# Optimization experiments

Hardware: AMD Instinct MI355X
Metric: run time of the kernel (lower is better)

## Reference

```python
import jax, jax.numpy as jnp
import numpy as np

B, L, DIM = 2, 2048, 2048
N_HEADS, N_KV_HEADS = 32, 8
HEAD_DIM = DIM // N_HEADS  # 64
SCALE = HEAD_DIM ** -0.5


def setup_inputs() -> dict:
    key = jax.random.key(0)
    ks = jax.random.split(key, 6)
    s = 0.02
    x = jax.random.normal(ks[0], (B, L, DIM), dtype=jnp.float32)
    wq = jax.random.normal(ks[1], (N_HEADS * HEAD_DIM, DIM), dtype=jnp.float32) * s
    wk = jax.random.normal(ks[2], (N_KV_HEADS * HEAD_DIM, DIM), dtype=jnp.float32) * s
    wv = jax.random.normal(ks[3], (N_KV_HEADS * HEAD_DIM, DIM), dtype=jnp.float32) * s
    wo = jax.random.normal(ks[4], (DIM, N_HEADS * HEAD_DIM), dtype=jnp.float32) * s
    # standard RoPE frequencies: theta = 10000^(-2i/d), angle = pos * theta
    inv_freq = 1.0 / (10000.0 ** (jnp.arange(0, HEAD_DIM, 2, dtype=jnp.float32) / HEAD_DIM))
    angles = jnp.arange(L, dtype=jnp.float32)[:, None] * inv_freq[None, :]  # [L, HEAD_DIM//2]
    freqs_cos = jnp.cos(angles)
    freqs_sin = jnp.sin(angles)
    # additive causal mask [1, 1, L, L]
    causal = jnp.tril(jnp.ones((L, L), dtype=bool))
    mask = jnp.where(causal, 0.0, -1e9).astype(jnp.float32)[None, None]
    return {"x": x, "wq": wq, "wk": wk, "wv": wv, "wo": wo,
            "freqs_cos": freqs_cos, "freqs_sin": freqs_sin, "mask": mask}


def _apply_rope(t, cos, sin):
    # t: [B, H, L, D]; complex pairing is (even, odd) interleaved along D
    te, to = t[..., 0::2], t[..., 1::2]
    cos = cos[None, None, : t.shape[2], :]
    sin = sin[None, None, : t.shape[2], :]
    re = te * cos - to * sin
    im = te * sin + to * cos
    return jnp.stack([re, im], axis=-1).reshape(t.shape)


def reference(x, wq, wk, wv, wo, freqs_cos, freqs_sin, mask):
    b, l, _ = x.shape
    q = (x @ wq.T).reshape(b, l, N_HEADS, HEAD_DIM).transpose(0, 2, 1, 3)
    k = (x @ wk.T).reshape(b, l, N_KV_HEADS, HEAD_DIM).transpose(0, 2, 1, 3)
    v = (x @ wv.T).reshape(b, l, N_KV_HEADS, HEAD_DIM).transpose(0, 2, 1, 3)
    q = _apply_rope(q, freqs_cos, freqs_sin)
    k = _apply_rope(k, freqs_cos, freqs_sin)
    repeats = N_HEADS // N_KV_HEADS
    k = jnp.repeat(k, repeats, axis=1)
    v = jnp.repeat(v, repeats, axis=1)
    scores = jnp.einsum("bhqd,bhkd->bhqk", q, k) * SCALE + mask
    probs = jax.nn.softmax(scores, axis=-1)
    out = jnp.einsum("bhqk,bhkd->bhqd", probs, v)
    out = out.transpose(0, 2, 1, 3).reshape(b, l, N_HEADS * HEAD_DIM)
    return out @ wo.T
```

## Files before the change

### kernel.cpp

```cpp
#include <hip/hip_runtime.h>
#include <hip/hip_bf16.h>
#include <stdint.h>

typedef __attribute__((ext_vector_type(8))) short bf16x8;
typedef __attribute__((ext_vector_type(4))) float f32x4;
typedef __attribute__((ext_vector_type(16))) float f32x16;
typedef __attribute__((ext_vector_type(4))) unsigned int u32x4;

#define B_    2
#define L_    2048
#define DIM_  2048
#define NH_   32
#define NKV_  8
#define HD_   64
#define KVD_  512
#define CLOG_ 0.1803368801111244f

__device__ __forceinline__ unsigned short f2bf(float f) {
  unsigned u = __float_as_uint(f);
  u += 0x7fff + ((u >> 16) & 1);
  return (unsigned short)(u >> 16);
}
__device__ __forceinline__ unsigned cvtpk(float lo, float hi_) {
  unsigned r;
  asm("v_cvt_pk_bf16_f32 %0, %1, %2" : "=v"(r) : "v"(lo), "v"(hi_));
  return r;
}

#define GLDS16(gsrc, ldst) __builtin_amdgcn_global_load_lds( \
    (const __attribute__((address_space(1))) unsigned int*)(gsrc), \
    (__attribute__((address_space(3))) unsigned int*)(ldst), 16, 0, 0)

__global__ void cvt_all(const float* __restrict__ x,  const float* __restrict__ wq,
                        const float* __restrict__ wk, const float* __restrict__ wv,
                        const float* __restrict__ wo,
                        unsigned short* __restrict__ xb,  unsigned short* __restrict__ wqb,
                        unsigned short* __restrict__ wkb, unsigned short* __restrict__ wvb,
                        unsigned short* __restrict__ wob) {
  int i = blockIdx.x * blockDim.x + threadIdx.x;
  const float* src; unsigned short* dst; int off;
  if (i < 2097152)      { src = x;  dst = xb;  off = i; }
  else if (i < 3145728) { src = wq; dst = wqb; off = i - 2097152; }
  else if (i < 3407872) { src = wk; dst = wkb; off = i - 3145728; }
  else if (i < 3670016) { src = wv; dst = wvb; off = i - 3407872; }
  else                  { src = wo; dst = wob; off = i - 3670016; }
  float4 v = reinterpret_cast<const float4*>(src)[off];
  ushort4 o;
  o.x = f2bf(v.x); o.y = f2bf(v.y); o.z = f2bf(v.z); o.w = f2bf(v.w);
  reinterpret_cast<ushort4*>(dst)[off] = o;
}

template<int OUT_F32>
__global__ __launch_bounds__(256) void gemm_bt(
    const unsigned short* __restrict__ A,
    const unsigned short* __restrict__ W,
    void* __restrict__ C, int M, int N, int K)
{
  __shared__ unsigned short As[128 * 64];
  __shared__ unsigned short Bs[128 * 64];
  const int tid = threadIdx.x;
  const int lane = tid & 63, wid = tid >> 6;
  const int wm = wid >> 1, wn = wid & 1;
  const int r = lane & 15, g = lane >> 4;
  const int m0 = blockIdx.y * 128, n0 = blockIdx.x * 128;
  f32x4 acc[4][4] = {};
  for (int k0 = 0; k0 < K; k0 += 64) {
#pragma unroll
    for (int p = 0; p < 4; ++p) {
      int off = (p * 256 + tid) * 16;
      int row = off >> 7, colb = off & 127;
      GLDS16((const char*)A + ((size_t)(m0 + row) * K + k0) * 2 + colb,
             (char*)As + off);
      GLDS16((const char*)W + ((size_t)(n0 + row) * K + k0) * 2 + colb,
             (char*)Bs + off);
    }
    __syncthreads();
#pragma unroll
    for (int kk = 0; kk < 2; ++kk) {
      bf16x8 af[4], bfv[4];
#pragma unroll
      for (int i = 0; i < 4; ++i)
        af[i] = *reinterpret_cast<const bf16x8*>(&As[(wm * 64 + i * 16 + r) * 64 + kk * 32 + g * 8]);
#pragma unroll
      for (int i = 0; i < 4; ++i)
        bfv[i] = *reinterpret_cast<const bf16x8*>(&Bs[(wn * 64 + i * 16 + r) * 64 + kk * 32 + g * 8]);
#pragma unroll
      for (int i = 0; i < 4; ++i)
#pragma unroll
        for (int j = 0; j < 4; ++j)
          acc[i][j] = __builtin_amdgcn_mfma_f32_16x16x32_bf16(af[i], bfv[j], acc[i][j], 0, 0, 0);
    }
    __syncthreads();
  }
#pragma unroll
  for (int i = 0; i < 4; ++i)
#pragma unroll
    for (int jf = 0; jf < 4; ++jf)
#pragma unroll
      for (int j = 0; j < 4; ++j) {
        size_t row = (size_t)(m0 + wm * 64 + i * 16 + g * 4 + j);
        size_t col = (size_t)(n0 + wn * 64 + jf * 16 + r);
        float v = acc[i][jf][j];
        if (OUT_F32) ((float*)C)[row * N + col] = v;
        else ((unsigned short*)C)[row * N + col] = f2bf(v);
      }
}

__global__ __launch_bounds__(256) void gemm_qkv(
    const unsigned short* __restrict__ A,
    const unsigned short* __restrict__ Wq,
    const unsigned short* __restrict__ Wk,
    const unsigned short* __restrict__ Wv,
    unsigned short* __restrict__ Cq,
    unsigned short* __restrict__ Ck,
    unsigned short* __restrict__ Cv)
{
  __shared__ unsigned short As[128 * 64];
  __shared__ unsigned short Bs[128 * 64];
  const int tid = threadIdx.x;
  const int lane = tid & 63, wid = tid >> 6;
  const int wm = wid >> 1, wn = wid & 1;
  const int r = lane & 15, g = lane >> 4;
  const int bx = blockIdx.x;
  const unsigned short* W; unsigned short* C; int N, n0;
  if (bx < 16)      { W = Wq; C = Cq; N = 2048; n0 = bx * 128; }
  else if (bx < 20) { W = Wk; C = Ck; N = 512;  n0 = (bx - 16) * 128; }
  else              { W = Wv; C = Cv; N = 512;  n0 = (bx - 20) * 128; }
  const int m0 = blockIdx.y * 128;
  const int K = DIM_;
  f32x4 acc[4][4] = {};
  for (int k0 = 0; k0 < K; k0 += 64) {
#pragma unroll
    for (int p = 0; p < 4; ++p) {
      int off = (p * 256 + tid) * 16;
      int row = off >> 7, colb = off & 127;
      GLDS16((const char*)A + ((size_t)(m0 + row) * K + k0) * 2 + colb,
             (char*)As + off);
      GLDS16((const char*)W + ((size_t)(n0 + row) * K + k0) * 2 + colb,
             (char*)Bs + off);
    }
    __syncthreads();
#pragma unroll
    for (int kk = 0; kk < 2; ++kk) {
      bf16x8 af[4], bfv[4];
#pragma unroll
      for (int i = 0; i < 4; ++i)
        af[i] = *reinterpret_cast<const bf16x8*>(&As[(wm * 64 + i * 16 + r) * 64 + kk * 32 + g * 8]);
#pragma unroll
      for (int i = 0; i < 4; ++i)
        bfv[i] = *reinterpret_cast<const bf16x8*>(&Bs[(wn * 64 + i * 16 + r) * 64 + kk * 32 + g * 8]);
#pragma unroll
      for (int i = 0; i < 4; ++i)
#pragma unroll
        for (int j = 0; j < 4; ++j)
          acc[i][j] = __builtin_amdgcn_mfma_f32_16x16x32_bf16(af[i], bfv[j], acc[i][j], 0, 0, 0);
    }
    __syncthreads();
  }
#pragma unroll
  for (int i = 0; i < 4; ++i)
#pragma unroll
    for (int jf = 0; jf < 4; ++jf)
#pragma unroll
      for (int j = 0; j < 4; ++j) {
        size_t row = (size_t)(m0 + wm * 64 + i * 16 + g * 4 + j);
        size_t col = (size_t)(n0 + wn * 64 + jf * 16 + r);
        C[row * N + col] = f2bf(acc[i][jf][j]);
      }
}

__global__ void rope_kernel(unsigned short* __restrict__ t,
                            const float* __restrict__ fc,
                            const float* __restrict__ fs, int rowElems,
                            float scale) {
  int p = blockIdx.x * blockDim.x + threadIdx.x;
  int pairsPerRow = rowElems >> 1;
  int row = p / pairsPerRow;
  if (row >= B_ * L_) return;
  int pi = p - row * pairsPerRow;
  int l = row & (L_ - 1);
  int h = pi >> 5, i = pi & 31;
  size_t base = (size_t)row * rowElems + h * 64 + 2 * i;
  float te = __uint_as_float(((unsigned)t[base]) << 16);
  float to = __uint_as_float(((unsigned)t[base + 1]) << 16);
  float c = fc[l * 32 + i] * scale, s = fs[l * 32 + i] * scale;
  t[base]     = f2bf(te * c - to * s);
  t[base + 1] = f2bf(te * s + to * c);
}

__global__ void transpose_v(const unsigned short* __restrict__ V,
                            unsigned short* __restrict__ Vt) {
  __shared__ unsigned short tile[64][65];
  int bkv = blockIdx.y;
  int b = bkv >> 3, kv = bkv & 7;
  int l0 = blockIdx.x * 64;
  int t = threadIdx.x;
#pragma unroll
  for (int it = 0; it < 16; ++it) {
    int idx = it * 256 + t;
    int lr = idx >> 6, dc = idx & 63;
    tile[lr][dc] = V[((size_t)(b * L_) + l0 + lr) * KVD_ + kv * HD_ + dc];
  }
  __syncthreads();
#pragma unroll
  for (int it = 0; it < 16; ++it) {
    int idx = it * 256 + t;
    int dr = idx >> 6, lc = idx & 63;
    Vt[(((size_t)(b * NKV_ + kv)) * HD_ + dr) * L_ + l0 + lc] = tile[lc][dr];
  }
}

__global__ __launch_bounds__(256) void attn_kernel(
    const unsigned short* __restrict__ Q,
    const unsigned short* __restrict__ K,
    const unsigned short* __restrict__ Vt,
    unsigned short* __restrict__ AO)
{
  __shared__ unsigned short Ks[2][64 * 64];
  __shared__ unsigned short Vs[2][64 * 64];
  const int tid = threadIdx.x;
  const int lane = tid & 63, w = tid >> 6;
  const int ql = lane & 31;
  const int hi = lane >> 5;
  const int wid = blockIdx.x;
  const int j = wid >> 6;
  const int blk = j >> 2, pos = j & 3;
  const int base = 15 - 4 * blk;
  const int qt = (blk & 1) ? (base - 3 + pos) : (base - pos);
  const int bh = wid & 63;
  const int b = bh >> 5, h = bh & 31, kv = h >> 2;
  const int q0 = qt * 128;
  const int qw = q0 + w * 32;
  const int nkt = (q0 + 128) >> 6;

  bf16x8 qf[4];
  const unsigned short* qbase = Q + ((size_t)(b * L_ + qw + ql)) * DIM_ + h * HD_ + hi * 8;
#pragma unroll
  for (int dk = 0; dk < 4; ++dk)
    qf[dk] = *reinterpret_cast<const bf16x8*>(qbase + dk * 16);

  const unsigned short* Kg = K + (size_t)b * L_ * KVD_ + kv * HD_;
  const unsigned short* Vg = Vt + ((size_t)(b * NKV_ + kv)) * HD_ * L_;

  f32x16 oacc0 = {}, oacc1 = {};
  float lrow = 0.f;
  const int rsw = (ql & 7) << 4;

  auto STAGE = [&](int buf, int t) {
    const int k0 = t * 64;
#pragma unroll
    for (int p = 0; p < 2; ++p) {
      int off = (p * 256 + tid) * 16;
      int row = off >> 7;
      int colb = (off & 127) ^ ((row & 7) << 4);
      GLDS16((const char*)Kg + ((size_t)(k0 + row)) * (KVD_ * 2) + colb,
             (char*)Ks[buf] + off);
      GLDS16((const char*)Vg + ((size_t)row) * (L_ * 2) + (size_t)k0 * 2 + colb,
             (char*)Vs[buf] + off);
    }
  };

  int cur = 0;
  STAGE(0, 0);
  __syncthreads();

  for (int t = 0; t < nkt; ++t) {
    if (t + 1 < nkt) STAGE(cur ^ 1, t + 1);
    const int k0 = t * 64;
    if (k0 < qw + 32) {
      const char* Kl = (const char*)Ks[cur];
      const char* Vl = (const char*)Vs[cur];
      f32x16 s0 = {}, s1 = {};
      __builtin_amdgcn_s_setprio(1);
#pragma unroll
      for (int dk = 0; dk < 4; ++dk) {
        bf16x8 kf0 = *reinterpret_cast<const bf16x8*>(Kl + ql * 128 + ((dk * 32 + hi * 16) ^ rsw));
        bf16x8 kf1 = *reinterpret_cast<const bf16x8*>(Kl + (32 + ql) * 128 + ((dk * 32 + hi * 16) ^ rsw));
        s0 = __builtin_amdgcn_mfma_f32_32x32x16_bf16(kf0, qf[dk], s0, 0, 0, 0);
        s1 = __builtin_amdgcn_mfma_f32_32x32x16_bf16(kf1, qf[dk], s1, 0, 0, 0);
      }
      __builtin_amdgcn_s_setprio(0);
      float p[32];
      float ps = 0.f;
      if (k0 + 63 > qw) {
        int q = qw + ql;
#pragma unroll
        for (int i = 0; i < 32; ++i) {
          float sv = (i < 16) ? s0[i] : s1[i - 16];
          int kk = k0 + (i >> 4) * 32 + (i & 3) + 8 * ((i & 15) >> 2) + 4 * hi;
          float e = exp2f(sv);
          e = (kk > q) ? 0.f : e;
          p[i] = e; ps += e;
        }
      } else {
#pragma unroll
        for (int i = 0; i < 32; ++i) {
          float sv = (i < 16) ? s0[i] : s1[i - 16];
          p[i] = exp2f(sv); ps += p[i];
        }
      }
      ps += __shfl_xor(ps, 32);
      lrow += ps;
      bf16x8 pf[4];
#pragma unroll
      for (int s = 0; s < 4; ++s) {
        int bp = ((s >> 1) << 4) + ((s & 1) << 3);
        unsigned w0 = cvtpk(p[bp + 0], p[bp + 1]);
        unsigned w1 = cvtpk(p[bp + 2], p[bp + 3]);
        unsigned w2 = cvtpk(p[bp + 4], p[bp + 5]);
        unsigned w3 = cvtpk(p[bp + 6], p[bp + 7]);
        unsigned x0 = (unsigned)__shfl_xor((int)w0, 32);
        unsigned x1 = (unsigned)__shfl_xor((int)w1, 32);
        unsigned x2 = (unsigned)__shfl_xor((int)w2, 32);
        unsigned x3 = (unsigned)__shfl_xor((int)w3, 32);
        u32x4 fw;
        fw[0] = hi ? x2 : w0;
        fw[1] = hi ? x3 : w1;
        fw[2] = hi ? w2 : x0;
        fw[3] = hi ? w3 : x1;
        pf[s] = __builtin_bit_cast(bf16x8, fw);
      }
      __builtin_amdgcn_s_setprio(1);
#pragma unroll
      for (int s = 0; s < 4; ++s) {
        bf16x8 v0 = *reinterpret_cast<const bf16x8*>(Vl + ql * 128 + ((s * 32 + hi * 16) ^ rsw));
        bf16x8 v1 = *reinterpret_cast<const bf16x8*>(Vl + (32 + ql) * 128 + ((s * 32 + hi * 16) ^ rsw));
        oacc0 = __builtin_amdgcn_mfma_f32_32x32x16_bf16(v0, pf[s], oacc0, 0, 0, 0);
        oacc1 = __builtin_amdgcn_mfma_f32_32x32x16_bf16(v1, pf[s], oacc1, 0, 0, 0);
      }
      __builtin_amdgcn_s_setprio(0);
    }
    __syncthreads();
    cur ^= 1;
  }

  float inv = 1.f / lrow;
  unsigned short* obase = AO + ((size_t)(b * L_ + qw + ql)) * DIM_ + h * HD_;
#pragma unroll
  for (int g4 = 0; g4 < 4; ++g4) {
    uint2 u;
    u.x = cvtpk(oacc0[g4 * 4 + 0] * inv, oacc0[g4 * 4 + 1] * inv);
    u.y = cvtpk(oacc0[g4 * 4 + 2] * inv, oacc0[g4 * 4 + 3] * inv);
    *reinterpret_cast<uint2*>(obase + g4 * 8 + hi * 4) = u;
    uint2 v;
    v.x = cvtpk(oacc1[g4 * 4 + 0] * inv, oacc1[g4 * 4 + 1] * inv);
    v.y = cvtpk(oacc1[g4 * 4 + 2] * inv, oacc1[g4 * 4 + 3] * inv);
    *reinterpret_cast<uint2*>(obase + 32 + g4 * 8 + hi * 4) = v;
  }
}

extern "C" void kernel_launch(void* const* d_in, const int* in_sizes, int n_in,
                              void* d_out, int out_size, void* d_ws, size_t ws_size,
                              hipStream_t stream) {
  const float* x  = (const float*)d_in[0];
  const float* wq = (const float*)d_in[1];
  const float* wk = (const float*)d_in[2];
  const float* wv = (const float*)d_in[3];
  const float* wo = (const float*)d_in[4];
  const float* fc = (const float*)d_in[5];
  const float* fs = (const float*)d_in[6];
  float* out = (float*)d_out;

  unsigned short* ws  = (unsigned short*)d_ws;
  unsigned short* xb  = ws;
  unsigned short* wqb = xb  + 8388608;
  unsigned short* wkb = wqb + 4194304;
  unsigned short* wvb = wkb + 1048576;
  unsigned short* wob = wvb + 1048576;
  unsigned short* Qb  = wob + 4194304;
  unsigned short* Kb  = Qb  + 8388608;
  unsigned short* Vb  = Kb  + 2097152;
  unsigned short* Vtb = Vb  + 2097152;
  unsigned short* AOb = Vtb + 2097152;

  cvt_all<<<18432, 256, 0, stream>>>(x, wq, wk, wv, wo, xb, wqb, wkb, wvb, wob);

  gemm_qkv<<<dim3(24, 32), 256, 0, stream>>>(xb, wqb, wkb, wvb, Qb, Kb, Vb);

  rope_kernel<<<16384, 256, 0, stream>>>(Qb, fc, fs, 2048, CLOG_);
  rope_kernel<<<4096,  256, 0, stream>>>(Kb, fc, fs, 512, 1.0f);

  transpose_v<<<dim3(32, 16), 256, 0, stream>>>(Vb, Vtb);

  attn_kernel<<<1024, 256, 0, stream>>>(Qb, Kb, Vtb, AOb);

  gemm_bt<1><<<dim3(16, 32), 256, 0, stream>>>(AOb, wob, out, 4096, 2048, 2048);
}
```

Baseline: 256.9 us.

## Rewrite projection GEMMs with 256x256 tiles, double-buffered LDS and swizzle

Replaces the 128x128 single-buffered bf16 GEMMs for the QKV and output projections with a shared 256x256-tile core running 512 threads. It double-buffers LDS so the next K slice loads while MFMAs run, XOR-swizzles LDS columns to avoid bank conflicts, and interleaves loads with compute using explicit waitcnt, barriers and setprio. The goal is higher arithmetic intensity and hidden global-load latency. In exchange it launches far fewer blocks (192 and 128), which can leave CUs idle, and uses much more LDS and registers per block.

```diff
diff --git a/kernel.cpp b/kernel.cpp
--- a/kernel.cpp
+++ b/kernel.cpp
@@ -30,6 +30,9 @@
 #define GLDS16(gsrc, ldst) __builtin_amdgcn_global_load_lds( \
     (const __attribute__((address_space(1))) unsigned int*)(gsrc), \
     (__attribute__((address_space(3))) unsigned int*)(ldst), 16, 0, 0)
+
+#define WAIT_LGKM0 asm volatile("s_waitcnt lgkmcnt(0)" ::: "memory")
+#define WAIT_VM0   asm volatile("s_waitcnt vmcnt(0)" ::: "memory")
 
 __global__ void cvt_all(const float* __restrict__ x,  const float* __restrict__ wq,
                         const float* __restrict__ wk, const float* __restrict__ wv,
@@ -51,62 +54,97 @@
 }
 
 template<int OUT_F32>
-__global__ __launch_bounds__(256) void gemm_bt(
+__device__ __forceinline__ void gemm256_core(
     const unsigned short* __restrict__ A,
     const unsigned short* __restrict__ W,
-    void* __restrict__ C, int M, int N, int K)
+    void* __restrict__ C, int N, int K, int m0, int n0,
+    unsigned short* As0, unsigned short* Bs0)
 {
-  __shared__ unsigned short As[128 * 64];
-  __shared__ unsigned short Bs[128 * 64];
+  unsigned short* As[2] = {As0, As0 + 256 * 64};
+  unsigned short* Bs[2] = {Bs0, Bs0 + 256 * 64};
   const int tid = threadIdx.x;
   const int lane = tid & 63, wid = tid >> 6;
-  const int wm = wid >> 1, wn = wid & 1;
+  const int wm = wid >> 2, wn = wid & 3;
   const int r = lane & 15, g = lane >> 4;
-  const int m0 = blockIdx.y * 128, n0 = blockIdx.x * 128;
-  f32x4 acc[4][4] = {};
-  for (int k0 = 0; k0 < K; k0 += 64) {
+  const int rsw = (r & 7) << 4;
+  const size_t rowbytes = (size_t)K * 2;
+
+  f32x4 acc[8][4] = {};
+
+  auto STAGEP = [&](int buf, int k0, int p) {
+    int off = (p * 512 + tid) * 16;
+    int row = off >> 7;
+    int colb = (off & 127) ^ ((row & 7) << 4);
+    GLDS16((const char*)A + (size_t)(m0 + row) * rowbytes + k0 * 2 + colb,
+           (char*)As[buf] + off);
+    GLDS16((const char*)W + (size_t)(n0 + row) * rowbytes + k0 * 2 + colb,
+           (char*)Bs[buf] + off);
+  };
+
+  const int nt = K >> 6;
+#pragma unroll
+  for (int p = 0; p < 4; ++p) STAGEP(0, 0, p);
+  WAIT_VM0;
+  __builtin_amdgcn_s_barrier();
+
+  for (int kt = 0; kt < nt; ++kt) {
+    const int cur = kt & 1;
+    const int k0 = kt << 6;
+    const bool hn = (kt + 1 < nt);
+    const char* Ab = (const char*)As[cur];
+    const char* Bb = (const char*)Bs[cur];
+    bf16x8 bfr[4][2];
 #pragma unroll
     for (int p = 0; p < 4; ++p) {
-      int off = (p * 256 + tid) * 16;
-      int row = off >> 7, colb = off & 127;
-      GLDS16((const char*)A + ((size_t)(m0 + row) * K + k0) * 2 + colb,
-             (char*)As + off);
-      GLDS16((const char*)W + ((size_t)(n0 + row) * K + k0) * 2 + colb,
-             (char*)Bs + off);
+      bf16x8 afr[2][2];
+      if (p == 0) {
+#pragma unroll
+        for (int ni = 0; ni < 4; ++ni)
+#pragma unroll
+          for (int kk = 0; kk < 2; ++kk)
+            bfr[ni][kk] = *reinterpret_cast<const bf16x8*>(
+                Bb + (wn * 64 + ni * 16 + r) * 128 + ((kk * 64 + g * 16) ^ rsw));
+      }
+#pragma unroll
+      for (int mi = 0; mi < 2; ++mi)
+#pragma unroll
+        for (int kk = 0; kk < 2; ++kk)
+          afr[mi][kk] = *reinterpret_cast<const bf16x8*>(
+              Ab + (wm * 128 + (p * 2 + mi) * 16 + r) * 128 + ((kk * 64 + g * 16) ^ rsw));
+      if (hn) STAGEP(cur ^ 1, k0 + 64, p);
+      __builtin_amdgcn_s_barrier();
+      WAIT_LGKM0;
+      __builtin_amdgcn_sched_barrier(0);
+      __builtin_amdgcn_s_setprio(1);
+#pragma unroll
+      for (int mi = 0; mi < 2; ++mi)
+#pragma unroll
+        for (int ni = 0; ni < 4; ++ni)
+#pragma unroll
+          for (int kk = 0; kk < 2; ++kk)
+            acc[p * 2 + mi][ni] = __builtin_amdgcn_mfma_f32_16x16x32_bf16(
+                afr[mi][kk], bfr[ni][kk], acc[p * 2 + mi][ni], 0, 0, 0);
+      __builtin_amdgcn_s_setprio(0);
+      if (p == 3) WAIT_VM0;
+      __builtin_amdgcn_s_barrier();
     }
-    __syncthreads();
-#pragma unroll
-    for (int kk = 0; kk < 2; ++kk) {
-      bf16x8 af[4], bfv[4];
-#pragma unroll
-      for (int i = 0; i < 4; ++i)
-        af[i] = *reinterpret_cast<const bf16x8*>(&As[(wm * 64 + i * 16 + r) * 64 + kk * 32 + g * 8]);
-#pragma unroll
-      for (int i = 0; i < 4; ++i)
-        bfv[i] = *reinterpret_cast<const bf16x8*>(&Bs[(wn * 64 + i * 16 + r) * 64 + kk * 32 + g * 8]);
-#pragma unroll
-      for (int i = 0; i < 4; ++i)
-#pragma unroll
-        for (int j = 0; j < 4; ++j)
-          acc[i][j] = __builtin_amdgcn_mfma_f32_16x16x32_bf16(af[i], bfv[j], acc[i][j], 0, 0, 0);
-    }
-    __syncthreads();
-  }
-#pragma unroll
-  for (int i = 0; i < 4; ++i)
-#pragma unroll
-    for (int jf = 0; jf < 4; ++jf)
+  }
+
+#pragma unroll
+  for (int mi = 0; mi < 8; ++mi)
+#pragma unroll
+    for (int ni = 0; ni < 4; ++ni)
 #pragma unroll
       for (int j = 0; j < 4; ++j) {
-        size_t row = (size_t)(m0 + wm * 64 + i * 16 + g * 4 + j);
-        size_t col = (size_t)(n0 + wn * 64 + jf * 16 + r);
-        float v = acc[i][jf][j];
+        size_t row = (size_t)(m0 + wm * 128 + mi * 16 + g * 4 + j);
+        size_t col = (size_t)(n0 + wn * 64 + ni * 16 + r);
+        float v = acc[mi][ni][j];
         if (OUT_F32) ((float*)C)[row * N + col] = v;
         else ((unsigned short*)C)[row * N + col] = f2bf(v);
       }
 }
 
-__global__ __launch_bounds__(256) void gemm_qkv(
+__global__ __launch_bounds__(512, 2) void gemm_qkv256(
     const unsigned short* __restrict__ A,
     const unsigned short* __restrict__ Wq,
     const unsigned short* __restrict__ Wk,
@@ -115,58 +153,24 @@
     unsigned short* __restrict__ Ck,
     unsigned short* __restrict__ Cv)
 {
-  __shared__ unsigned short As[128 * 64];
-  __shared__ unsigned short Bs[128 * 64];
-  const int tid = threadIdx.x;
-  const int lane = tid & 63, wid = tid >> 6;
-  const int wm = wid >> 1, wn = wid & 1;
-  const int r = lane & 15, g = lane >> 4;
+  __shared__ unsigned short As[2 * 256 * 64];
+  __shared__ unsigned short Bs[2 * 256 * 64];
   const int bx = blockIdx.x;
   const unsigned short* W; unsigned short* C; int N, n0;
-  if (bx < 16)      { W = Wq; C = Cq; N = 2048; n0 = bx * 128; }
-  else if (bx < 20) { W = Wk; C = Ck; N = 512;  n0 = (bx - 16) * 128; }
-  else              { W = Wv; C = Cv; N = 512;  n0 = (bx - 20) * 128; }
-  const int m0 = blockIdx.y * 128;
-  const int K = DIM_;
-  f32x4 acc[4][4] = {};
-  for (int k0 = 0; k0 < K; k0 += 64) {
-#pragma unroll
-    for (int p = 0; p < 4; ++p) {
-      int off = (p * 256 + tid) * 16;
-      int row = off >> 7, colb = off & 127;
-      GLDS16((const char*)A + ((size_t)(m0 + row) * K + k0) * 2 + colb,
-             (char*)As + off);
-      GLDS16((const char*)W + ((size_t)(n0 + row) * K + k0) * 2 + colb,
-             (char*)Bs + off);
-    }
-    __syncthreads();
-#pragma unroll
-    for (int kk = 0; kk < 2; ++kk) {
-      bf16x8 af[4], bfv[4];
-#pragma unroll
-      for (int i = 0; i < 4; ++i)
-        af[i] = *reinterpret_cast<const bf16x8*>(&As[(wm * 64 + i * 16 + r) * 64 + kk * 32 + g * 8]);
-#pragma unroll
-      for (int i = 0; i < 4; ++i)
-        bfv[i] = *reinterpret_cast<const bf16x8*>(&Bs[(wn * 64 + i * 16 + r) * 64 + kk * 32 + g * 8]);
-#pragma unroll
-      for (int i = 0; i < 4; ++i)
-#pragma unroll
-        for (int j = 0; j < 4; ++j)
-          acc[i][j] = __builtin_amdgcn_mfma_f32_16x16x32_bf16(af[i], bfv[j], acc[i][j], 0, 0, 0);
-    }
-    __syncthreads();
-  }
-#pragma unroll
-  for (int i = 0; i < 4; ++i)
-#pragma unroll
-    for (int jf = 0; jf < 4; ++jf)
-#pragma unroll
-      for (int j = 0; j < 4; ++j) {
-        size_t row = (size_t)(m0 + wm * 64 + i * 16 + g * 4 + j);
-        size_t col = (size_t)(n0 + wn * 64 + jf * 16 + r);
-        C[row * N + col] = f2bf(acc[i][jf][j]);
-      }
+  if (bx < 8)       { W = Wq; C = Cq; N = 2048; n0 = bx * 256; }
+  else if (bx < 10) { W = Wk; C = Ck; N = 512;  n0 = (bx - 8) * 256; }
+  else              { W = Wv; C = Cv; N = 512;  n0 = (bx - 10) * 256; }
+  gemm256_core<0>(A, W, C, N, DIM_, blockIdx.y * 256, n0, As, Bs);
+}
+
+__global__ __launch_bounds__(512, 2) void gemm_out256(
+    const unsigned short* __restrict__ A,
+    const unsigned short* __restrict__ W,
+    float* __restrict__ C)
+{
+  __shared__ unsigned short As[2 * 256 * 64];
+  __shared__ unsigned short Bs[2 * 256 * 64];
+  gemm256_core<1>(A, W, C, DIM_, DIM_, blockIdx.y * 256, blockIdx.x * 256, As, Bs);
 }
 
 __global__ void rope_kernel(unsigned short* __restrict__ t,
@@ -375,7 +379,7 @@
 
   cvt_all<<<18432, 256, 0, stream>>>(x, wq, wk, wv, wo, xb, wqb, wkb, wvb, wob);
 
-  gemm_qkv<<<dim3(24, 32), 256, 0, stream>>>(xb, wqb, wkb, wvb, Qb, Kb, Vb);
+  gemm_qkv256<<<dim3(12, 16), 512, 0, stream>>>(xb, wqb, wkb, wvb, Qb, Kb, Vb);
 
   rope_kernel<<<16384, 256, 0, stream>>>(Qb, fc, fs, 2048, CLOG_);
   rope_kernel<<<4096,  256, 0, stream>>>(Kb, fc, fs, 512, 1.0f);
@@ -384,5 +388,5 @@
 
   attn_kernel<<<1024, 256, 0, stream>>>(Qb, Kb, Vtb, AOb);
 
-  gemm_bt<1><<<dim3(16, 32), 256, 0, stream>>>(AOb, wob, out, 4096, 2048, 2048);
-}
+  gemm_out256<<<dim3(8, 16), 512, 0, stream>>>(AOb, wob, out);
+}
```

Result: slower. 359.2 us (+39.8%).
